# Kernel tuning notes

Measured on AMD Instinct MI355X. Metric: run time of the kernel, lower is better.

The kernel has to match this reference:

```python
import jax, jax.numpy as jnp
import numpy as np

F = 64        # atom feature dim (from Linear(64, 32))
N_RBF = 25    # Gaussian RBF expansion size (standard SchNet 0..5 A)
CUTOFF = 5.0
GAMMA = 10.0  # RBF width parameter: exp(-gamma * (d - mu)^2)


def ssp(x):
    # shifted softplus: ln(0.5 * e^x + 0.5) = softplus(x) - ln 2
    return jax.nn.softplus(x) - jnp.log(2.0).astype(x.dtype)


def setup_inputs() -> dict:
    key = jax.random.key(0)
    ks = jax.random.split(key, 16)
    B, N = 4, 512
    embedding = jax.random.normal(ks[0], (B, N, F), jnp.float32)
    d = jax.random.uniform(ks[1], (B, N, N), jnp.float32) * CUTOFF
    distances = 0.5 * (d + jnp.swapaxes(d, 1, 2))  # symmetric pairwise distances
    s = 0.1
    # 3 stacked interaction blocks
    in2f = jax.random.normal(ks[2], (3, F, F), jnp.float32) * s      # atomwise in->filter (no bias)
    fw1 = jax.random.normal(ks[3], (3, N_RBF, F), jnp.float32) * s   # filter net layer 1
    fb1 = jnp.zeros((3, F), jnp.float32)
    fw2 = jax.random.normal(ks[4], (3, F, F), jnp.float32) * s       # filter net layer 2
    fb2 = jnp.zeros((3, F), jnp.float32)
    f2o = jax.random.normal(ks[5], (3, F, F), jnp.float32) * s       # filter->out atomwise
    f2b = jnp.zeros((3, F), jnp.float32)
    dw = jax.random.normal(ks[6], (3, F, F), jnp.float32) * s        # output atomwise
    db = jnp.zeros((3, F), jnp.float32)
    # readout MLP: Linear(64,32) + SSP + Linear(32,1)
    aw1 = jax.random.normal(ks[7], (F, 32), jnp.float32) * s
    ab1 = jnp.zeros((32,), jnp.float32)
    aw2 = jax.random.normal(ks[8], (32, 1), jnp.float32) * s
    ab2 = jnp.zeros((1,), jnp.float32)
    return dict(embedding=embedding, distances=distances, in2f=in2f, fw1=fw1,
                fb1=fb1, fw2=fw2, fb2=fb2, f2o=f2o, f2b=f2b, dw=dw, db=db,
                aw1=aw1, ab1=ab1, aw2=aw2, ab2=ab2)


def reference(embedding, distances, in2f, fw1, fb1, fw2, fb2, f2o, f2b, dw, db,
              aw1, ab1, aw2, ab2):
    dtype = embedding.dtype
    centers = jnp.linspace(0.0, CUTOFF, N_RBF).astype(dtype)
    # Gaussian RBF expansion of pairwise distances: [B, N, N, N_RBF]
    rbf = jnp.exp(-GAMMA * jnp.square(distances[..., None] - centers))
    x = embedding  # [B, N, F]
    for i in range(3):
        f = x @ in2f[i]  # [B, N, F]
        # filter-generating network on expanded distances -> [B, N, N, F]
        W = ssp(jnp.einsum('bijr,rf->bijf', rbf, fw1[i]) + fb1[i])
        W = W @ fw2[i] + fb2[i]
        # continuous-filter convolution: y_i = sum_j f_j * W_ij
        y = jnp.einsum('bjf,bijf->bif', f, W)
        y = ssp(y @ f2o[i] + f2b[i])
        y = y @ dw[i] + db[i]
        x = x + y  # residual
    h = ssp(x @ aw1 + ab1)   # [B, N, 32]
    return h @ aw2 + ab2     # [B, N, 1]
```

## Files before the change

kernel.cpp:

```cpp
#include <hip/hip_runtime.h>

#define KBIN 160
#define TSTRIDE 68
#define TPSZ  10880
#define FBASE 10880
#define FB2   14976

typedef _Float16 half2v __attribute__((ext_vector_type(2)));

__device__ __forceinline__ float ssp(float x) {
    return fmaxf(x, 0.0f) + log1pf(expf(-fabsf(x))) - 0.69314718055994531f;
}

__device__ __forceinline__ float bclane(float v, int l) {
    return __builtin_bit_cast(float, __builtin_amdgcn_readlane(__builtin_bit_cast(int, v), l));
}

__device__ __forceinline__ unsigned int kaenc(float d) {
    float tv = fminf(fmaxf(d, 0.0f)*32.0f, 159.999f);
    int k = (int)tv;
    float fr = tv - (float)k;
    unsigned short fh = __builtin_bit_cast(unsigned short, (_Float16)fr);
    return ((unsigned int)(k*272) << 16) | (unsigned int)fh;
}

__device__ __forceinline__ float matvec64(const float* __restrict__ ldsA, int base, float xv, int lane) {
    float a0 = 0.f, a1 = 0.f, a2 = 0.f, a3 = 0.f;
    #pragma unroll
    for (int gg = 0; gg < 16; ++gg) {
        const float4 w = *(const float4*)&ldsA[base + lane*64 + (((gg + lane) & 15) << 2)];
        a0 += bclane(xv, gg*4+0) * w.x;
        a1 += bclane(xv, gg*4+1) * w.y;
        a2 += bclane(xv, gg*4+2) * w.z;
        a3 += bclane(xv, gg*4+3) * w.w;
    }
    return (a0 + a1) + (a2 + a3);
}

__device__ __forceinline__ void matvec64x2(const float* __restrict__ ldsA, int base,
                                           float xv0, float xv1, int lane,
                                           float& o0, float& o1) {
    float a0 = 0.f, a1 = 0.f, b0 = 0.f, b1 = 0.f;
    #pragma unroll
    for (int gg = 0; gg < 16; ++gg) {
        const float4 w = *(const float4*)&ldsA[base + lane*64 + (((gg + lane) & 15) << 2)];
        a0 += bclane(xv0, gg*4+0) * w.x;
        a1 += bclane(xv0, gg*4+1) * w.y;
        a0 += bclane(xv0, gg*4+2) * w.z;
        a1 += bclane(xv0, gg*4+3) * w.w;
        b0 += bclane(xv1, gg*4+0) * w.x;
        b1 += bclane(xv1, gg*4+1) * w.y;
        b0 += bclane(xv1, gg*4+2) * w.z;
        b1 += bclane(xv1, gg*4+3) * w.w;
    }
    o0 = a0 + a1;
    o1 = b0 + b1;
}

__device__ __forceinline__ void stageWT(float* __restrict__ lds, int base, const float* __restrict__ W, int tid) {
    for (int s = tid; s < 4096; s += 512) {
        int f = s >> 6, g = s & 63;
        lds[base + g*64 + ((((f >> 2) + g) & 15) << 2) + (f & 3)] = W[s];
    }
}

__global__ __launch_bounds__(512) void schnet_pre0(
    const float* __restrict__ emb, const float* __restrict__ dists,
    const float* __restrict__ in2f,
    const float* __restrict__ fw1, const float* __restrict__ fb1,
    const float* __restrict__ fw2, const float* __restrict__ fb2,
    unsigned short* __restrict__ f_out, unsigned int* __restrict__ Tp_g,
    unsigned int* __restrict__ ka)
{
    __shared__ float lds[12544];
    const int wg = blockIdx.x, tid = threadIdx.x;
    const int wave = tid >> 6, lane = tid & 63;
    if (wg < 128) {
        stageWT(lds, 0, in2f, tid);
        __syncthreads();
        int row0 = wg*16 + wave*2;
        size_t ro0 = (size_t)row0*64 + lane;
        size_t ro1 = ro0 + 64;
        float f0, f1;
        matvec64x2(lds, 0, emb[ro0], emb[ro1], lane, f0, f1);
        f_out[ro0] = __builtin_bit_cast(unsigned short, (_Float16)f0);
        f_out[ro1] = __builtin_bit_cast(unsigned short, (_Float16)f1);
    } else if (wg < 188) {
        int widx = wg - 128;
        int tt = widx / 20;
        int k = (widx % 20)*8 + wave;
        const float* fw1t = fw1 + tt*25*64;
        const float* fw2t = fw2 + tt*64*64;
        for (int s = tid; s < 1600; s += 512) lds[s] = fw1t[s];
        for (int s = tid; s < 4096; s += 512) lds[1600 + s] = fw2t[s];
        if (tid < 64) { lds[5696 + tid] = fb1[tt*64 + tid]; lds[5760 + tid] = fb2[tt*64 + tid]; }
        __syncthreads();
        float T2[2];
        #pragma unroll
        for (int e = 0; e < 2; ++e) {
            float dk = (float)(k + e) * (5.0f/160.0f);
            float h1 = lds[5696 + lane];
            for (int r = 0; r < 25; ++r) {
                float sr = dk - (float)r * (5.0f/24.0f);
                h1 += expf(-10.0f*sr*sr) * lds[r*64 + lane];
            }
            float u = ssp(h1);
            float T = lds[5760 + lane];
            #pragma unroll
            for (int gg = 0; gg < 64; ++gg)
                T += bclane(u, gg) * lds[1600 + gg*64 + lane];
            T2[e] = T;
        }
        float* sc = &lds[5824 + wave*128];
        sc[lane] = T2[0];
        sc[64 + lane] = T2[1];
        if (lane < 16) {
            float4 A  = *(const float4*)&sc[lane*4];
            float4 Bv = *(const float4*)&sc[64 + lane*4];
            half2v t01 = { (_Float16)A.x, (_Float16)A.y };
            half2v t23 = { (_Float16)A.z, (_Float16)A.w };
            half2v d01 = { (_Float16)(Bv.x - A.x), (_Float16)(Bv.y - A.y) };
            half2v d23 = { (_Float16)(Bv.z - A.z), (_Float16)(Bv.w - A.w) };
            uint4 o;
            o.x = __builtin_bit_cast(unsigned int, t01);
            o.y = __builtin_bit_cast(unsigned int, t23);
            o.z = __builtin_bit_cast(unsigned int, d01);
            o.w = __builtin_bit_cast(unsigned int, d23);
            *(uint4*)&Tp_g[(size_t)tt*TPSZ + k*TSTRIDE + lane*4] = o;
        }
    } else {
        size_t p = (size_t)(wg - 188)*4096 + (size_t)tid*8;
        float4 d0 = *(const float4*)&dists[p];
        float4 d1 = *(const float4*)&dists[p + 4];
        uint4 o0, o1;
        o0.x = kaenc(d0.x); o0.y = kaenc(d0.y); o0.z = kaenc(d0.z); o0.w = kaenc(d0.w);
        o1.x = kaenc(d1.x); o1.y = kaenc(d1.y); o1.z = kaenc(d1.z); o1.w = kaenc(d1.w);
        *(uint4*)&ka[p] = o0;
        *(uint4*)&ka[p + 4] = o1;
    }
}

__global__ __launch_bounds__(512, 4) void schnet_block(
    int t,
    const float* __restrict__ emb,
    const float* __restrict__ in2f,
    const float* __restrict__ f2o, const float* __restrict__ f2b,
    const float* __restrict__ dw,  const float* __restrict__ db,
    const float* __restrict__ aw1, const float* __restrict__ ab1,
    const float* __restrict__ aw2, const float* __restrict__ ab2,
    const unsigned int* __restrict__ Tp_g,
    const unsigned int* __restrict__ ka,
    const unsigned short* __restrict__ f_in,
    unsigned short* __restrict__ f_out,
    float* __restrict__ x_buf, float* __restrict__ out)
{
    __shared__ unsigned int ldsu[FB2 + 4096];
    float* lds = (float*)ldsu;
    const int wg = blockIdx.x, tid = threadIdx.x;
    const int wave = tid >> 6, lane = tid & 63;
    const int b = wg >> 7, it = wg & 127;
    const int i0 = it * 4;
    const int fq = lane & 15, g = lane >> 4;
    const int r = wave >> 1;
    const int jhalf = wave & 1;

    const unsigned int* Tp = Tp_g + (size_t)t*TPSZ;
    for (int s = tid; s < TPSZ/4; s += 512)
        ((uint4*)ldsu)[s] = ((const uint4*)Tp)[s];

    const int j0 = tid >> 4, fq2 = tid & 15;
    const uint2* fsrc0 = (const uint2*)f_in + ((size_t)b*512 + j0)*16 + fq2;
    const int fo_base = (j0 >> 1)*64 + fq2*4 + (j0 & 1)*2;
    unsigned int* fdstA = ldsu + FBASE + fo_base;
    unsigned int* fdstB = ldsu + FB2 + fo_base;
    const unsigned int* kabase = &ka[((size_t)(b*512 + i0 + r))*512 + jhalf*64 + g*16];

    uint2 rb0, rb1, rb2, rb3;
    uint4 kc0, kc1, kc2, kc3, kn0, kn1, kn2, kn3;
    {
        rb0 = fsrc0[0]; rb1 = fsrc0[512]; rb2 = fsrc0[1024]; rb3 = fsrc0[1536];
        kc0 = ((const uint4*)kabase)[0];
        kc1 = ((const uint4*)kabase)[1];
        kc2 = ((const uint4*)kabase)[2];
        kc3 = ((const uint4*)kabase)[3];
        *(uint2*)fdstA = rb0; *(uint2*)(fdstA + 1024) = rb1;
        *(uint2*)(fdstA + 2048) = rb2; *(uint2*)(fdstA + 3072) = rb3;
    }
    __syncthreads();

    const unsigned int* fpA = ldsu + FBASE + fq*4;
    const unsigned int* fpB = ldsu + FB2 + fq*4;
    const char* Tbyte = (const char*)ldsu + fq*16;
    const int jpb = jhalf*32 + g*8;
    float a0 = 0.f, a1 = 0.f, a2 = 0.f, a3 = 0.f;

    #pragma unroll
    for (int c = 0; c < 4; ++c) {
        if (c < 3) {
            const uint2* sp = fsrc0 + (size_t)(c + 1)*2048;
            rb0 = sp[0]; rb1 = sp[512]; rb2 = sp[1024]; rb3 = sp[1536];
            const uint4* kp = (const uint4*)(kabase + (c + 1)*128);
            kn0 = kp[0]; kn1 = kp[1]; kn2 = kp[2]; kn3 = kp[3];
        }
        const unsigned int* fp = (c & 1) ? fpB : fpA;
        uint4 kqa[4] = {kc0, kc1, kc2, kc3};
        #pragma unroll
        for (int j4 = 0; j4 < 4; ++j4) {
            uint4 fA = *(const uint4*)&fp[(jpb + j4*2)*64];
            uint4 fB = *(const uint4*)&fp[(jpb + j4*2 + 1)*64];
            unsigned int kk[4] = {kqa[j4].x, kqa[j4].y, kqa[j4].z, kqa[j4].w};
            unsigned int fl_[8] = {fA.x, fA.y, fA.z, fA.w, fB.x, fB.y, fB.z, fB.w};
            #pragma unroll
            for (int u = 0; u < 4; ++u) {
                unsigned int kau = kk[u];
                unsigned int koff = kau >> 16;
                half2v av = __builtin_bit_cast(half2v, __builtin_amdgcn_perm(kau, kau, 0x01000100u));
                uint4 tp = *(const uint4*)(Tbyte + koff);
                half2v W01 = __builtin_bit_cast(half2v, tp.z)*av + __builtin_bit_cast(half2v, tp.x);
                half2v W23 = __builtin_bit_cast(half2v, tp.w)*av + __builtin_bit_cast(half2v, tp.y);
                half2v f01 = __builtin_bit_cast(half2v, fl_[u*2]);
                half2v f23 = __builtin_bit_cast(half2v, fl_[u*2+1]);
                a0 += (float)W01[0] * (float)f01[0];
                a1 += (float)W01[1] * (float)f01[1];
                a2 += (float)W23[0] * (float)f23[0];
                a3 += (float)W23[1] * (float)f23[1];
            }
        }
        if (c < 3) {
            unsigned int* fd = (c & 1) ? fdstA : fdstB;
            *(uint2*)fd = rb0; *(uint2*)(fd + 1024) = rb1;
            *(uint2*)(fd + 2048) = rb2; *(uint2*)(fd + 3072) = rb3;
            kc0 = kn0; kc1 = kn1; kc2 = kn2; kc3 = kn3;
            __syncthreads();
        }
    }
    a0 += __shfl_xor(a0, 16, 64); a0 += __shfl_xor(a0, 32, 64);
    a1 += __shfl_xor(a1, 16, 64); a1 += __shfl_xor(a1, 32, 64);
    a2 += __shfl_xor(a2, 16, 64); a2 += __shfl_xor(a2, 32, 64);
    a3 += __shfl_xor(a3, 16, 64); a3 += __shfl_xor(a3, 32, 64);

    __syncthreads();
    if (g == 0) {
        float4 acc; acc.x = a0; acc.y = a1; acc.z = a2; acc.w = a3;
        *(float4*)&lds[FB2 + wave*64 + fq*4] = acc;
    }
    stageWT(lds, 0, f2o + t*4096, tid);
    stageWT(lds, 4096, dw + t*4096, tid);
    if (t < 2) {
        stageWT(lds, 8192, in2f + (t+1)*4096, tid);
    } else {
        for (int s = tid; s < 4096; s += 512) {
            int f = s >> 6, rr = s & 63;
            lds[8192 + rr*64 + ((((f >> 2) + rr) & 15) << 2) + (f & 3)] = aw1[f*32 + (rr & 31)];
        }
    }
    if (tid < 64) {
        lds[12288 + tid] = f2b[t*64 + tid];
        lds[12352 + tid] = db[t*64 + tid];
        if (t == 2) {
            lds[12416 + tid] = ab1[tid & 31];
            lds[12480 + tid] = aw2[tid & 31];
        }
    }
    __syncthreads();

    if (wave < 4) {
        int grow = b*512 + i0 + wave;
        size_t ro = (size_t)grow*64 + lane;
        float y = lds[FB2 + (wave*2)*64 + lane] + lds[FB2 + (wave*2+1)*64 + lane];
        float z = matvec64(lds, 0, y, lane) + lds[12288 + lane];
        float u = ssp(z);
        float y3 = matvec64(lds, 4096, u, lane) + lds[12352 + lane];
        float xin = (t == 0) ? emb[ro] : x_buf[ro];
        float xn = xin + y3;
        if (t < 2) {
            x_buf[ro] = xn;
            float fo = matvec64(lds, 8192, xn, lane);
            f_out[ro] = __builtin_bit_cast(unsigned short, (_Float16)fo);
        } else {
            float s1 = matvec64(lds, 8192, xn, lane) + lds[12416 + lane];
            float h = ssp(s1) * lds[12480 + lane];
            #pragma unroll
            for (int m = 1; m < 64; m <<= 1)
                h += __shfl_xor(h, m, 64);
            if (lane == 0) out[grow] = ab2[0] + 0.5f*h;
        }
    }
}

extern "C" void kernel_launch(void* const* d_in, const int* in_sizes, int n_in,
                              void* d_out, int out_size, void* d_ws, size_t ws_size,
                              hipStream_t stream) {
    const float* emb  = (const float*)d_in[0];
    const float* dist = (const float*)d_in[1];
    const float* in2f = (const float*)d_in[2];
    const float* fw1  = (const float*)d_in[3];
    const float* fb1  = (const float*)d_in[4];
    const float* fw2  = (const float*)d_in[5];
    const float* fb2  = (const float*)d_in[6];
    const float* f2o  = (const float*)d_in[7];
    const float* f2b  = (const float*)d_in[8];
    const float* dwp  = (const float*)d_in[9];
    const float* dbp  = (const float*)d_in[10];
    const float* aw1  = (const float*)d_in[11];
    const float* ab1  = (const float*)d_in[12];
    const float* aw2  = (const float*)d_in[13];
    const float* ab2  = (const float*)d_in[14];
    float* out = (float*)d_out;
    float* ws = (float*)d_ws;
    unsigned int* Tp_g = (unsigned int*)ws;
    unsigned short* fA = (unsigned short*)(ws + 32640);
    unsigned short* fB = (unsigned short*)(ws + 32640 + 65536);
    float* x_buf = ws + 32640 + 2*65536;
    unsigned int* ka = (unsigned int*)(x_buf + 131072);

    hipLaunchKernelGGL(schnet_pre0, dim3(444), dim3(512), 0, stream,
        emb, dist, in2f, fw1, fb1, fw2, fb2, fA, Tp_g, ka);
    hipLaunchKernelGGL(schnet_block, dim3(512), dim3(512), 0, stream,
        0, emb, in2f, f2o, f2b, dwp, dbp, aw1, ab1, aw2, ab2,
        Tp_g, ka, fA, fB, x_buf, out);
    hipLaunchKernelGGL(schnet_block, dim3(512), dim3(512), 0, stream,
        1, emb, in2f, f2o, f2b, dwp, dbp, aw1, ab1, aw2, ab2,
        Tp_g, ka, fB, fA, x_buf, out);
    hipLaunchKernelGGL(schnet_block, dim3(512), dim3(512), 0, stream,
        2, emb, in2f, f2o, f2b, dwp, dbp, aw1, ab1, aw2, ab2,
        Tp_g, ka, fA, fB, x_buf, out);
}
```

Measured before the change: 65.27 us.

## Fuse distance encoding into first block, shrink filter table, vectorize weight staging

Moves the per-pair distance encoding out of the precompute kernel and into the first interaction-block launch, where each workgroup encodes its own rows before reading them back. This removes the large extra grid from the precompute kernel. It also shrinks the tabulated filter from 160 to 128 distance bins, which cuts table size and LDS footprint but makes the interpolation grid coarser and may reduce accuracy. Weight transposes into LDS now use float4 stores instead of scalar stores.

After: 61.81 us. 1.06x faster.

```diff
diff --git a/kernel.cpp b/kernel.cpp
--- a/kernel.cpp
+++ b/kernel.cpp
@@ -1,10 +1,10 @@
 #include <hip/hip_runtime.h>
 
-#define KBIN 160
+#define KBIN 128
 #define TSTRIDE 68
-#define TPSZ  10880
-#define FBASE 10880
-#define FB2   14976
+#define TPSZ  8704
+#define FBASE 8704
+#define FB2   12800
 
 typedef _Float16 half2v __attribute__((ext_vector_type(2)));
 
@@ -17,7 +17,7 @@
 }
 
 __device__ __forceinline__ unsigned int kaenc(float d) {
-    float tv = fminf(fmaxf(d, 0.0f)*32.0f, 159.999f);
+    float tv = fminf(fmaxf(d, 0.0f)*25.6f, 127.999f);
     int k = (int)tv;
     float fr = tv - (float)k;
     unsigned short fh = __builtin_bit_cast(unsigned short, (_Float16)fr);
@@ -57,26 +57,30 @@
     o1 = b0 + b1;
 }
 
-__device__ __forceinline__ void stageWT(float* __restrict__ lds, int base, const float* __restrict__ W, int tid) {
-    for (int s = tid; s < 4096; s += 512) {
-        int f = s >> 6, g = s & 63;
-        lds[base + g*64 + ((((f >> 2) + g) & 15) << 2) + (f & 3)] = W[s];
+__device__ __forceinline__ void stageWT4(float* __restrict__ lds, int base, const float* __restrict__ W, int tid) {
+    for (int s = tid; s < 1024; s += 512) {
+        int quad = s >> 6, g = s & 63;
+        float4 v;
+        v.x = W[(quad*4+0)*64 + g];
+        v.y = W[(quad*4+1)*64 + g];
+        v.z = W[(quad*4+2)*64 + g];
+        v.w = W[(quad*4+3)*64 + g];
+        *(float4*)&lds[base + g*64 + (((quad + g) & 15) << 2)] = v;
     }
 }
 
 __global__ __launch_bounds__(512) void schnet_pre0(
-    const float* __restrict__ emb, const float* __restrict__ dists,
+    const float* __restrict__ emb,
     const float* __restrict__ in2f,
     const float* __restrict__ fw1, const float* __restrict__ fb1,
     const float* __restrict__ fw2, const float* __restrict__ fb2,
-    unsigned short* __restrict__ f_out, unsigned int* __restrict__ Tp_g,
-    unsigned int* __restrict__ ka)
+    unsigned short* __restrict__ f_out, unsigned int* __restrict__ Tp_g)
 {
     __shared__ float lds[12544];
     const int wg = blockIdx.x, tid = threadIdx.x;
     const int wave = tid >> 6, lane = tid & 63;
     if (wg < 128) {
-        stageWT(lds, 0, in2f, tid);
+        stageWT4(lds, 0, in2f, tid);
         __syncthreads();
         int row0 = wg*16 + wave*2;
         size_t ro0 = (size_t)row0*64 + lane;
@@ -85,10 +89,10 @@
         matvec64x2(lds, 0, emb[ro0], emb[ro1], lane, f0, f1);
         f_out[ro0] = __builtin_bit_cast(unsigned short, (_Float16)f0);
         f_out[ro1] = __builtin_bit_cast(unsigned short, (_Float16)f1);
-    } else if (wg < 188) {
+    } else {
         int widx = wg - 128;
-        int tt = widx / 20;
-        int k = (widx % 20)*8 + wave;
+        int tt = widx / 16;
+        int k = (widx % 16)*8 + wave;
         const float* fw1t = fw1 + tt*25*64;
         const float* fw2t = fw2 + tt*64*64;
         for (int s = tid; s < 1600; s += 512) lds[s] = fw1t[s];
@@ -98,7 +102,7 @@
         float T2[2];
         #pragma unroll
         for (int e = 0; e < 2; ++e) {
-            float dk = (float)(k + e) * (5.0f/160.0f);
+            float dk = (float)(k + e) * (5.0f/128.0f);
             float h1 = lds[5696 + lane];
             for (int r = 0; r < 25; ++r) {
                 float sr = dk - (float)r * (5.0f/24.0f);
@@ -128,28 +132,19 @@
             o.w = __builtin_bit_cast(unsigned int, d23);
             *(uint4*)&Tp_g[(size_t)tt*TPSZ + k*TSTRIDE + lane*4] = o;
         }
-    } else {
-        size_t p = (size_t)(wg - 188)*4096 + (size_t)tid*8;
-        float4 d0 = *(const float4*)&dists[p];
-        float4 d1 = *(const float4*)&dists[p + 4];
-        uint4 o0, o1;
-        o0.x = kaenc(d0.x); o0.y = kaenc(d0.y); o0.z = kaenc(d0.z); o0.w = kaenc(d0.w);
-        o1.x = kaenc(d1.x); o1.y = kaenc(d1.y); o1.z = kaenc(d1.z); o1.w = kaenc(d1.w);
-        *(uint4*)&ka[p] = o0;
-        *(uint4*)&ka[p + 4] = o1;
     }
 }
 
 __global__ __launch_bounds__(512, 4) void schnet_block(
     int t,
-    const float* __restrict__ emb,
+    const float* __restrict__ emb, const float* __restrict__ dists,
     const float* __restrict__ in2f,
     const float* __restrict__ f2o, const float* __restrict__ f2b,
     const float* __restrict__ dw,  const float* __restrict__ db,
     const float* __restrict__ aw1, const float* __restrict__ ab1,
     const float* __restrict__ aw2, const float* __restrict__ ab2,
     const unsigned int* __restrict__ Tp_g,
-    const unsigned int* __restrict__ ka,
+    unsigned int* __restrict__ ka,
     const unsigned short* __restrict__ f_in,
     unsigned short* __restrict__ f_out,
     float* __restrict__ x_buf, float* __restrict__ out)
@@ -168,6 +163,16 @@
     for (int s = tid; s < TPSZ/4; s += 512)
         ((uint4*)ldsu)[s] = ((const uint4*)Tp)[s];
 
+    if (t == 0) {
+        int erow = tid >> 7;
+        int ecol = (tid & 127) * 4;
+        size_t ep = ((size_t)(b*512 + i0 + erow))*512 + ecol;
+        float4 dv = *(const float4*)&dists[ep];
+        uint4 eo;
+        eo.x = kaenc(dv.x); eo.y = kaenc(dv.y); eo.z = kaenc(dv.z); eo.w = kaenc(dv.w);
+        *(uint4*)&ka[ep] = eo;
+    }
+
     const int j0 = tid >> 4, fq2 = tid & 15;
     const uint2* fsrc0 = (const uint2*)f_in + ((size_t)b*512 + j0)*16 + fq2;
     const int fo_base = (j0 >> 1)*64 + fq2*4 + (j0 & 1)*2;
@@ -179,14 +184,22 @@
     uint4 kc0, kc1, kc2, kc3, kn0, kn1, kn2, kn3;
     {
         rb0 = fsrc0[0]; rb1 = fsrc0[512]; rb2 = fsrc0[1024]; rb3 = fsrc0[1536];
+        if (t > 0) {
+            kc0 = ((const uint4*)kabase)[0];
+            kc1 = ((const uint4*)kabase)[1];
+            kc2 = ((const uint4*)kabase)[2];
+            kc3 = ((const uint4*)kabase)[3];
+        }
+        *(uint2*)fdstA = rb0; *(uint2*)(fdstA + 1024) = rb1;
+        *(uint2*)(fdstA + 2048) = rb2; *(uint2*)(fdstA + 3072) = rb3;
+    }
+    __syncthreads();
+    if (t == 0) {
         kc0 = ((const uint4*)kabase)[0];
         kc1 = ((const uint4*)kabase)[1];
         kc2 = ((const uint4*)kabase)[2];
         kc3 = ((const uint4*)kabase)[3];
-        *(uint2*)fdstA = rb0; *(uint2*)(fdstA + 1024) = rb1;
-        *(uint2*)(fdstA + 2048) = rb2; *(uint2*)(fdstA + 3072) = rb3;
-    }
-    __syncthreads();
+    }
 
     const unsigned int* fpA = ldsu + FBASE + fq*4;
     const unsigned int* fpB = ldsu + FB2 + fq*4;
@@ -244,14 +257,19 @@
         float4 acc; acc.x = a0; acc.y = a1; acc.z = a2; acc.w = a3;
         *(float4*)&lds[FB2 + wave*64 + fq*4] = acc;
     }
-    stageWT(lds, 0, f2o + t*4096, tid);
-    stageWT(lds, 4096, dw + t*4096, tid);
+    stageWT4(lds, 0, f2o + t*4096, tid);
+    stageWT4(lds, 4096, dw + t*4096, tid);
     if (t < 2) {
-        stageWT(lds, 8192, in2f + (t+1)*4096, tid);
+        stageWT4(lds, 8192, in2f + (t+1)*4096, tid);
     } else {
-        for (int s = tid; s < 4096; s += 512) {
-            int f = s >> 6, rr = s & 63;
-            lds[8192 + rr*64 + ((((f >> 2) + rr) & 15) << 2) + (f & 3)] = aw1[f*32 + (rr & 31)];
+        for (int s = tid; s < 1024; s += 512) {
+            int quad = s >> 6, rr = s & 63;
+            float4 v;
+            v.x = aw1[(quad*4+0)*32 + (rr & 31)];
+            v.y = aw1[(quad*4+1)*32 + (rr & 31)];
+            v.z = aw1[(quad*4+2)*32 + (rr & 31)];
+            v.w = aw1[(quad*4+3)*32 + (rr & 31)];
+            *(float4*)&lds[8192 + rr*64 + (((quad + rr) & 15) << 2)] = v;
         }
     }
     if (tid < 64) {
@@ -309,20 +327,20 @@
     float* out = (float*)d_out;
     float* ws = (float*)d_ws;
     unsigned int* Tp_g = (unsigned int*)ws;
-    unsigned short* fA = (unsigned short*)(ws + 32640);
-    unsigned short* fB = (unsigned short*)(ws + 32640 + 65536);
-    float* x_buf = ws + 32640 + 2*65536;
+    unsigned short* fA = (unsigned short*)(ws + 26112);
+    unsigned short* fB = (unsigned short*)(ws + 26112 + 65536);
+    float* x_buf = ws + 26112 + 2*65536;
     unsigned int* ka = (unsigned int*)(x_buf + 131072);
 
-    hipLaunchKernelGGL(schnet_pre0, dim3(444), dim3(512), 0, stream,
-        emb, dist, in2f, fw1, fb1, fw2, fb2, fA, Tp_g, ka);
+    hipLaunchKernelGGL(schnet_pre0, dim3(176), dim3(512), 0, stream,
+        emb, in2f, fw1, fb1, fw2, fb2, fA, Tp_g);
     hipLaunchKernelGGL(schnet_block, dim3(512), dim3(512), 0, stream,
-        0, emb, in2f, f2o, f2b, dwp, dbp, aw1, ab1, aw2, ab2,
+        0, emb, dist, in2f, f2o, f2b, dwp, dbp, aw1, ab1, aw2, ab2,
         Tp_g, ka, fA, fB, x_buf, out);
     hipLaunchKernelGGL(schnet_block, dim3(512), dim3(512), 0, stream,
-        1, emb, in2f, f2o, f2b, dwp, dbp, aw1, ab1, aw2, ab2,
+        1, emb, dist, in2f, f2o, f2b, dwp, dbp, aw1, ab1, aw2, ab2,
         Tp_g, ka, fB, fA, x_buf, out);
     hipLaunchKernelGGL(schnet_block, dim3(512), dim3(512), 0, stream,
-        2, emb, in2f, f2o, f2b, dwp, dbp, aw1, ab1, aw2, ab2,
+        2, emb, dist, in2f, f2o, f2b, dwp, dbp, aw1, ab1, aw2, ab2,
         Tp_g, ka, fA, fB, x_buf, out);
 }
```
